# Kernel optimization log

Hardware: AMD Instinct MI355X
Metric: run time of the kernel (lower is better)

Reference implementation:

```python
import jax, jax.numpy as jnp
import numpy as np

N, E, IN, H, OUT = 100000, 1600000, 128, 128, 64


def setup_inputs() -> dict:
    key = jax.random.key(0)
    ks = jax.random.split(key, 6)
    glorot = lambda k, i, o: jax.random.normal(k, (i, o), jnp.float32) * np.float32(np.sqrt(2.0 / (i + o)))
    return dict(
        x=jax.random.normal(ks[0], (N, IN), jnp.float32),
        edge_index=jax.random.randint(ks[1], (2, E), 0, N, dtype=jnp.int64 if jax.config.jax_enable_x64 else jnp.int32),
        W1=glorot(ks[2], IN, H), b1=jnp.zeros((H,), jnp.float32),
        W2=glorot(ks[3], H, H), b2=jnp.zeros((H,), jnp.float32),
        W3=glorot(ks[4], H, OUT), b3=jnp.zeros((OUT,), jnp.float32),
    )


def _gcn_norm(edge_index, num_nodes):
    # add self loops with weight 1.0 (GCNConv add_self_loops=True, edge_weight=None -> ones)
    loop = jnp.arange(num_nodes, dtype=edge_index.dtype)
    src = jnp.concatenate([edge_index[0], loop])
    dst = jnp.concatenate([edge_index[1], loop])
    ew = jnp.ones(src.shape, jnp.float32)
    deg = jax.ops.segment_sum(ew, dst, num_segments=num_nodes)  # in-degree on dst
    dinv = jnp.where(deg > 0, jax.lax.rsqrt(deg), 0.0)
    norm = dinv[src] * ew * dinv[dst]  # [E+N]
    return src, dst, norm


def _conv(x, src, dst, norm, W, b):
    h = x @ W                                        # linear transform first (GCNConv order)
    msg = h[src] * norm[:, None]                     # gather + scale, [E+N, F]
    agg = jax.ops.segment_sum(msg, dst, num_segments=x.shape[0])  # scatter-add
    return agg + b


def reference(x, edge_index, W1, b1, W2, b2, W3, b3):
    # eval-mode forward: dropout is identity
    src, dst, norm = _gcn_norm(edge_index, x.shape[0])  # same graph -> norm shared across layers
    h = jax.nn.relu(_conv(x, src, dst, norm, W1, b1))
    h = jax.nn.relu(_conv(h, src, dst, norm, W2, b2))
    h = _conv(h, src, dst, norm, W3, b3)
    return jax.nn.log_softmax(h, axis=-1)
```

## Files before the change

### kernel.cpp

```cpp
#include <hip/hip_runtime.h>

typedef unsigned int u32;
typedef unsigned short u16;
typedef unsigned char u8;
typedef __attribute__((ext_vector_type(8))) short short8;
typedef __attribute__((ext_vector_type(4))) float f32x4;
typedef __attribute__((ext_vector_type(2))) float f32x2;

#define MAXBIN 1024

__device__ inline float bfu2f(u32 u) { return __builtin_bit_cast(float, u); }
__device__ inline u16 f2bf(float f) {
    u32 u = __builtin_bit_cast(u32, f);
    u32 r = (u + 0x7fffu + ((u >> 16) & 1u)) >> 16;
    return (u16)r;
}

__global__ __launch_bounds__(256) void k_bhist(const int* __restrict__ ei, int E, int W,
                                               int* __restrict__ binTot, int NBIN) {
    __shared__ int h[MAXBIN];
    int tid = threadIdx.x;
    for (int i = tid; i < NBIN; i += 256) h[i] = 0;
    __syncthreads();
    int s = blockIdx.x * W, e = min(E, s + W);
    for (int j = s + tid; j < e; j += 256) atomicAdd(&h[ei[E + j] >> 7], 1);
    __syncthreads();
    for (int i = tid; i < NBIN; i += 256) {
        int v = h[i];
        if (v) atomicAdd(&binTot[i], v);
    }
}

__global__ void k_bscan(const int* __restrict__ binTot, int NBIN,
                        int* __restrict__ binStart, int* __restrict__ binCur) {
    __shared__ int wsum[4];
    int t = threadIdx.x;
    int base = t * 4;
    int v0 = (base + 0 < NBIN) ? binTot[base + 0] : 0;
    int v1 = (base + 1 < NBIN) ? binTot[base + 1] : 0;
    int v2 = (base + 2 < NBIN) ? binTot[base + 2] : 0;
    int v3 = (base + 3 < NBIN) ? binTot[base + 3] : 0;
    int s = v0 + v1 + v2 + v3;
    int lane = t & 63, wv = t >> 6;
    int isc = s;
    for (int d = 1; d < 64; d <<= 1) { int o = __shfl_up(isc, d, 64); if (lane >= d) isc += o; }
    if (lane == 63) wsum[wv] = isc;
    __syncthreads();
    int woff = 0;
    for (int w = 0; w < wv; w++) woff += wsum[w];
    int run = woff + isc - s;
    if (base + 0 < NBIN) { binStart[base + 0] = run; binCur[base + 0] = run; } run += v0;
    if (base + 1 < NBIN) { binStart[base + 1] = run; binCur[base + 1] = run; } run += v1;
    if (base + 2 < NBIN) { binStart[base + 2] = run; binCur[base + 2] = run; } run += v2;
    if (base + 3 < NBIN) { binStart[base + 3] = run; binCur[base + 3] = run; }
    if (t == 255) binStart[NBIN] = wsum[0] + wsum[1] + wsum[2] + wsum[3];
}

__global__ __launch_bounds__(256) void k_bscatter(const int* __restrict__ ei, int E, int W,
                                                  int* __restrict__ binCur,
                                                  u32* __restrict__ binned, int NBIN) {
    __shared__ int lh[MAXBIN];
    __shared__ int lb[MAXBIN];
    int tid = threadIdx.x;
    for (int i = tid; i < NBIN; i += 256) lh[i] = 0;
    __syncthreads();
    int s = blockIdx.x * W, e = min(E, s + W);
    for (int j = s + tid; j < e; j += 256) atomicAdd(&lh[ei[E + j] >> 7], 1);
    __syncthreads();
    for (int i = tid; i < NBIN; i += 256) {
        int h = lh[i];
        lb[i] = h ? atomicAdd(&binCur[i], h) : 0;
    }
    __syncthreads();
    for (int i = tid; i < NBIN; i += 256) lh[i] = 0;
    __syncthreads();
    for (int j = s + tid; j < e; j += 256) {
        int d = ei[E + j];
        int b = d >> 7;
        int r = atomicAdd(&lh[b], 1);
        binned[lb[b] + r] = ((u32)ei[j] << 7) | (u32)(d & 127);
    }
}

__global__ __launch_bounds__(256) void k_bcsr(const u32* __restrict__ binned,
                                              const int* __restrict__ binStart,
                                              int N, int E, int* __restrict__ offs,
                                              float* __restrict__ dinv,
                                              int* __restrict__ csr, int NBIN) {
    __shared__ int cnt[128];
    __shared__ int off[128];
    __shared__ int tot;
    int b = blockIdx.x;
    int tid = threadIdx.x;
    int dLo = b << 7;
    int nd = min(128, N - dLo);
    int e0 = binStart[b], e1 = binStart[b + 1];
    if (tid < 128) cnt[tid] = 0;
    __syncthreads();
    for (int j = e0 + tid; j < e1; j += 256) atomicAdd(&cnt[binned[j] & 127u], 1);
    __syncthreads();
    int c = (tid < 128) ? cnt[tid] : 0;
    int lane = tid & 63;
    int isc = c;
    for (int d = 1; d < 64; d <<= 1) { int o = __shfl_up(isc, d, 64); if (lane >= d) isc += o; }
    if (tid == 63) tot = isc;
    __syncthreads();
    int add = (tid >= 64 && tid < 128) ? tot : 0;
    if (tid < 128) off[tid] = add + isc - c;
    __syncthreads();
    if (tid < nd) {
        offs[dLo + tid] = e0 + off[tid];
        dinv[dLo + tid] = rsqrtf((float)(c + 1));
    }
    if (b == NBIN - 1 && tid == 0) offs[N] = E;
    if (tid < 128) cnt[tid] = 0;
    __syncthreads();
    for (int j = e0 + tid; j < e1; j += 256) {
        u32 v = binned[j];
        int d7 = (int)(v & 127u);
        int r = atomicAdd(&cnt[d7], 1);
        csr[e0 + off[d7] + r] = (int)(v >> 7);
    }
}

__global__ void k_wtall(const float* __restrict__ W1, const float* __restrict__ W2,
                        const float* __restrict__ W3, u16* __restrict__ wt1,
                        u16* __restrict__ wt2, u16* __restrict__ wt3) {
    int idx = blockIdx.x * 256 + threadIdx.x;
    if (idx < 16384) {
        int k = idx >> 7, m = idx & 127;
        wt1[m * 128 + k] = f2bf(W1[idx]);
    } else if (idx < 32768) {
        int i = idx - 16384, k = i >> 7, m = i & 127;
        wt2[m * 128 + k] = f2bf(W2[i]);
    } else if (idx < 40960) {
        int i = idx - 32768, k = i >> 6, m = i & 63;
        wt3[m * 128 + k] = f2bf(W3[i]);
    }
}

template <int M, bool F32IN>
__global__ __launch_bounds__(256) void k_gemm(const void* __restrict__ xin,
                                              const u16* __restrict__ wt,
                                              const float* __restrict__ dinv,
                                              u8* __restrict__ g8, int N) {
    constexpr int K = 128;
    constexpr int LDK = 136;
    __shared__ u16 lwt[M * LDK];
    int tid = threadIdx.x;
    const uint4* wsrc = (const uint4*)wt;
#pragma unroll
    for (int c = tid; c < M * K / 8; c += 256) {
        int row = c >> 4, kc = c & 15;
        *(uint4*)&lwt[row * LDK + kc * 8] = wsrc[c];
    }
    __syncthreads();
    int lane = tid & 63, wv = tid >> 6;
    int node = blockIdx.x * 64 + wv * 16 + (lane & 15);
    int nodec = min(node, N - 1);
    int kr = (lane >> 4) * 8;
    f32x4 acc[M / 16];
#pragma unroll
    for (int t = 0; t < M / 16; t++) acc[t] = (f32x4){0.f, 0.f, 0.f, 0.f};
#pragma unroll
    for (int ks = 0; ks < 4; ks++) {
        short8 bfr;
        if (F32IN) {
            const float* xr = (const float*)xin + (size_t)nodec * K + ks * 32 + kr;
            float4 fa = *(const float4*)xr;
            float4 fb = *(const float4*)(xr + 4);
            bfr = (short8){(short)f2bf(fa.x), (short)f2bf(fa.y), (short)f2bf(fa.z),
                           (short)f2bf(fa.w), (short)f2bf(fb.x), (short)f2bf(fb.y),
                           (short)f2bf(fb.z), (short)f2bf(fb.w)};
        } else {
            bfr = *(const short8*)((const u16*)xin + (size_t)nodec * K + ks * 32 + kr);
        }
#pragma unroll
        for (int t = 0; t < M / 16; t++) {
            short8 afr = *(const short8*)&lwt[(t * 16 + (lane & 15)) * LDK + ks * 32 + kr];
            acc[t] = __builtin_amdgcn_mfma_f32_16x16x32_bf16(afr, bfr, acc[t], 0, 0, 0);
        }
    }
    if (node < N) {
        float dv16 = dinv[node] * 16.0f;
        int r0 = (lane >> 4) * 4;
#pragma unroll
        for (int t = 0; t < M / 16; t++) {
            u32 w = __builtin_amdgcn_cvt_pk_fp8_f32(acc[t][0] * dv16, acc[t][1] * dv16, 0, false);
            w = __builtin_amdgcn_cvt_pk_fp8_f32(acc[t][2] * dv16, acc[t][3] * dv16, w, true);
            *(u32*)(g8 + (size_t)node * M + t * 16 + r0) = w;
        }
    }
}

__global__ __launch_bounds__(256) void k_agg128(const u8* __restrict__ g8,
                                                const int* __restrict__ offs,
                                                const int* __restrict__ csr,
                                                const float* __restrict__ dinv,
                                                const float* __restrict__ bias,
                                                u16* __restrict__ hout, int N) {
    int wid = (blockIdx.x * 256 + threadIdx.x) >> 6;
    if (wid >= N) return;
    int lane = threadIdx.x & 63;
    int q = lane >> 4;
    int f = lane & 15;
    int s = offs[wid], e = offs[wid + 1];
    const u8* gf = g8 + f * 8;
    f32x2 a01 = {0.f, 0.f}, a23 = {0.f, 0.f}, a45 = {0.f, 0.f}, a67 = {0.f, 0.f};
    int em1 = e - 1;
    for (int j = s; j < e; j += 16) {
        int b4 = j + q * 4;
        int i1 = b4 + 1, i2 = b4 + 2, i3 = b4 + 3;
        int s0 = csr[min(b4, em1)];
        int s1 = csr[min(i1, em1)];
        int s2 = csr[min(i2, em1)];
        int s3 = csr[min(i3, em1)];
        uint2 w0 = *(const uint2*)(gf + ((u32)s0 << 7));
        uint2 w1 = *(const uint2*)(gf + ((u32)s1 << 7));
        uint2 w2 = *(const uint2*)(gf + ((u32)s2 << 7));
        uint2 w3 = *(const uint2*)(gf + ((u32)s3 << 7));
        if (b4 >= e) { w0.x = 0u; w0.y = 0u; }
        if (i1 >= e) { w1.x = 0u; w1.y = 0u; }
        if (i2 >= e) { w2.x = 0u; w2.y = 0u; }
        if (i3 >= e) { w3.x = 0u; w3.y = 0u; }
        f32x2 t0, t1;
        t0 = __builtin_amdgcn_cvt_pk_f32_fp8((int)w0.x, false) +
             __builtin_amdgcn_cvt_pk_f32_fp8((int)w1.x, false);
        t1 = __builtin_amdgcn_cvt_pk_f32_fp8((int)w2.x, false) +
             __builtin_amdgcn_cvt_pk_f32_fp8((int)w3.x, false);
        a01 += t0 + t1;
        t0 = __builtin_amdgcn_cvt_pk_f32_fp8((int)w0.x, true) +
             __builtin_amdgcn_cvt_pk_f32_fp8((int)w1.x, true);
        t1 = __builtin_amdgcn_cvt_pk_f32_fp8((int)w2.x, true) +
             __builtin_amdgcn_cvt_pk_f32_fp8((int)w3.x, true);
        a23 += t0 + t1;
        t0 = __builtin_amdgcn_cvt_pk_f32_fp8((int)w0.y, false) +
             __builtin_amdgcn_cvt_pk_f32_fp8((int)w1.y, false);
        t1 = __builtin_amdgcn_cvt_pk_f32_fp8((int)w2.y, false) +
             __builtin_amdgcn_cvt_pk_f32_fp8((int)w3.y, false);
        a45 += t0 + t1;
        t0 = __builtin_amdgcn_cvt_pk_f32_fp8((int)w0.y, true) +
             __builtin_amdgcn_cvt_pk_f32_fp8((int)w1.y, true);
        t1 = __builtin_amdgcn_cvt_pk_f32_fp8((int)w2.y, true) +
             __builtin_amdgcn_cvt_pk_f32_fp8((int)w3.y, true);
        a67 += t0 + t1;
    }
    float a[8] = {a01.x, a01.y, a23.x, a23.y, a45.x, a45.y, a67.x, a67.y};
#pragma unroll
    for (int i = 0; i < 8; i++) {
        a[i] += __shfl_xor(a[i], 16, 64);
        a[i] += __shfl_xor(a[i], 32, 64);
    }
    if (lane < 16) {
        float sc = dinv[wid] * 0.0625f;
        uint2 sp = *(const uint2*)(g8 + (size_t)wid * 128 + f * 8);
        f32x2 s01 = __builtin_amdgcn_cvt_pk_f32_fp8((int)sp.x, false);
        f32x2 s23 = __builtin_amdgcn_cvt_pk_f32_fp8((int)sp.x, true);
        f32x2 s45 = __builtin_amdgcn_cvt_pk_f32_fp8((int)sp.y, false);
        f32x2 s67 = __builtin_amdgcn_cvt_pk_f32_fp8((int)sp.y, true);
        float sv[8] = {s01.x, s01.y, s23.x, s23.y, s45.x, s45.y, s67.x, s67.y};
        float4 b0 = *(const float4*)(bias + f * 8);
        float4 b1 = *(const float4*)(bias + f * 8 + 4);
        float bv[8] = {b0.x, b0.y, b0.z, b0.w, b1.x, b1.y, b1.z, b1.w};
        u32 o[4];
#pragma unroll
        for (int i = 0; i < 4; i++) {
            float v0 = fmaxf(fmaf(a[2 * i] + sv[2 * i], sc, bv[2 * i]), 0.f);
            float v1 = fmaxf(fmaf(a[2 * i + 1] + sv[2 * i + 1], sc, bv[2 * i + 1]), 0.f);
            o[i] = (u32)f2bf(v0) | ((u32)f2bf(v1) << 16);
        }
        *(uint4*)&hout[(size_t)wid * 128 + f * 8] = make_uint4(o[0], o[1], o[2], o[3]);
    }
}

__global__ __launch_bounds__(256) void k_agg64(const u8* __restrict__ g8,
                                               const int* __restrict__ offs,
                                               const int* __restrict__ csr,
                                               const float* __restrict__ dinv,
                                               const float* __restrict__ bias,
                                               float* __restrict__ out, int N) {
    int wid = (blockIdx.x * 256 + threadIdx.x) >> 6;
    if (wid >= N) return;
    int lane = threadIdx.x & 63;
    int q = lane >> 4;
    int f = lane & 15;
    int s = offs[wid], e = offs[wid + 1];
    const u8* gf = g8 + f * 4;
    f32x2 a01 = {0.f, 0.f}, a23 = {0.f, 0.f};
    int em1 = e - 1;
    for (int j = s; j < e; j += 16) {
        int b4 = j + q * 4;
        int i1 = b4 + 1, i2 = b4 + 2, i3 = b4 + 3;
        int s0 = csr[min(b4, em1)];
        int s1 = csr[min(i1, em1)];
        int s2 = csr[min(i2, em1)];
        int s3 = csr[min(i3, em1)];
        u32 w0 = *(const u32*)(gf + ((u32)s0 << 6));
        u32 w1 = *(const u32*)(gf + ((u32)s1 << 6));
        u32 w2 = *(const u32*)(gf + ((u32)s2 << 6));
        u32 w3 = *(const u32*)(gf + ((u32)s3 << 6));
        if (b4 >= e) w0 = 0u;
        if (i1 >= e) w1 = 0u;
        if (i2 >= e) w2 = 0u;
        if (i3 >= e) w3 = 0u;
        f32x2 t0 = __builtin_amdgcn_cvt_pk_f32_fp8((int)w0, false) +
                   __builtin_amdgcn_cvt_pk_f32_fp8((int)w1, false);
        f32x2 t1 = __builtin_amdgcn_cvt_pk_f32_fp8((int)w2, false) +
                   __builtin_amdgcn_cvt_pk_f32_fp8((int)w3, false);
        a01 += t0 + t1;
        t0 = __builtin_amdgcn_cvt_pk_f32_fp8((int)w0, true) +
             __builtin_amdgcn_cvt_pk_f32_fp8((int)w1, true);
        t1 = __builtin_amdgcn_cvt_pk_f32_fp8((int)w2, true) +
             __builtin_amdgcn_cvt_pk_f32_fp8((int)w3, true);
        a23 += t0 + t1;
    }
    float a[4] = {a01.x, a01.y, a23.x, a23.y};
#pragma unroll
    for (int i = 0; i < 4; i++) {
        a[i] += __shfl_xor(a[i], 16, 64);
        a[i] += __shfl_xor(a[i], 32, 64);
    }
    if (lane < 16) {
        float sc = dinv[wid] * 0.0625f;
        u32 sp = *(const u32*)(g8 + (size_t)wid * 64 + f * 4);
        f32x2 s01 = __builtin_amdgcn_cvt_pk_f32_fp8((int)sp, false);
        f32x2 s23 = __builtin_amdgcn_cvt_pk_f32_fp8((int)sp, true);
        float4 bb = *(const float4*)(bias + f * 4);
        float v0 = fmaf(a[0] + s01.x, sc, bb.x);
        float v1 = fmaf(a[1] + s01.y, sc, bb.y);
        float v2 = fmaf(a[2] + s23.x, sc, bb.z);
        float v3 = fmaf(a[3] + s23.y, sc, bb.w);
        float m = fmaxf(fmaxf(v0, v1), fmaxf(v2, v3));
#pragma unroll
        for (int d = 8; d >= 1; d >>= 1) m = fmaxf(m, __shfl_xor(m, d, 64));
        float ssum = __expf(v0 - m) + __expf(v1 - m) + __expf(v2 - m) + __expf(v3 - m);
#pragma unroll
        for (int d = 8; d >= 1; d >>= 1) ssum += __shfl_xor(ssum, d, 64);
        float lg = m + __logf(ssum);
        *(float4*)&out[(size_t)wid * 64 + f * 4] =
            make_float4(v0 - lg, v1 - lg, v2 - lg, v3 - lg);
    }
}

extern "C" void kernel_launch(void* const* d_in, const int* in_sizes, int n_in,
                              void* d_out, int out_size, void* d_ws, size_t ws_size,
                              hipStream_t stream) {
    const float* x  = (const float*)d_in[0];
    const int*   ei = (const int*)d_in[1];
    const float* W1 = (const float*)d_in[2];
    const float* b1 = (const float*)d_in[3];
    const float* W2 = (const float*)d_in[4];
    const float* b2 = (const float*)d_in[5];
    const float* W3 = (const float*)d_in[6];
    const float* b3 = (const float*)d_in[7];
    const int N = in_sizes[0] / 128;
    const int E = in_sizes[1] / 2;
    const int NBIN = (N + 127) >> 7;

    char* ws = (char*)d_ws;
    size_t o = 0;
    auto alloc = [&](size_t bytes) -> char* {
        char* p = ws + o;
        o += (bytes + 255) & ~(size_t)255;
        return p;
    };
    int*   binTot = (int*)alloc((size_t)MAXBIN * 4);
    int*   binSt  = (int*)alloc((size_t)(MAXBIN + 1) * 4);
    int*   binCur = (int*)alloc((size_t)MAXBIN * 4);
    float* dinv   = (float*)alloc((size_t)N * 4);
    int*   offs   = (int*)alloc((size_t)(N + 1) * 4);
    int*   csr    = (int*)alloc((size_t)E * 4);
    u16*   wt1    = (u16*)alloc(128 * 128 * 2);
    u16*   wt2    = (u16*)alloc(128 * 128 * 2);
    u16*   wt3    = (u16*)alloc(64 * 128 * 2);
    u8*    g8     = (u8*)alloc((size_t)N * 128);
    u16*   hbuf   = (u16*)alloc((size_t)N * 128 * 2);
    u32*   binned = (u32*)hbuf;
    float* outp   = (float*)d_out;

    hipMemsetAsync(binTot, 0, (size_t)MAXBIN * 4, stream);
    int W256 = (E + 255) / 256;
    int W128 = (E + 127) / 128;
    k_bhist<<<256, 256, 0, stream>>>(ei, E, W256, binTot, NBIN);
    k_bscan<<<1, 256, 0, stream>>>(binTot, NBIN, binSt, binCur);
    k_bscatter<<<128, 256, 0, stream>>>(ei, E, W128, binCur, binned, NBIN);
    k_bcsr<<<NBIN, 256, 0, stream>>>(binned, binSt, N, E, offs, dinv, csr, NBIN);
    k_wtall<<<(40960 + 255) / 256, 256, 0, stream>>>(W1, W2, W3, wt1, wt2, wt3);

    int gG = (N + 63) / 64;
    int gA = (int)(((size_t)N * 64 + 255) / 256);

    k_gemm<128, true ><<<gG, 256, 0, stream>>>(x,    wt1, dinv, g8, N);
    k_agg128<<<gA, 256, 0, stream>>>(g8, offs, csr, dinv, b1, hbuf, N);
    k_gemm<128, false><<<gG, 256, 0, stream>>>(hbuf, wt2, dinv, g8, N);
    k_agg128<<<gA, 256, 0, stream>>>(g8, offs, csr, dinv, b2, hbuf, N);
    k_gemm<64,  false><<<gG, 256, 0, stream>>>(hbuf, wt3, dinv, g8, N);
    k_agg64<<<gA, 256, 0, stream>>>(g8, offs, csr, dinv, b3, outp, N);
}
```

Before: 346.8 us.

## Replace two-level binned CSR build with global-atomic degree count and scatter

Replaces the bucketed CSR construction (LDS histogram, bin scan, bin scatter, per-bin local sort) with a direct approach: global atomic degree counts, a two-pass block scan to compute row offsets, and a global-atomic scatter of source indices into CSR slots. This drops the intermediate binned array and a pass over the edges, but relies on contended global atomics across 100k nodes. The order of neighbours within a row becomes nondeterministic, which changes the float summation order in aggregation. k_offs assumes NB <= 256 for the block-prefix reduction.

```diff
diff --git a/kernel.cpp b/kernel.cpp
--- a/kernel.cpp
+++ b/kernel.cpp
@@ -7,8 +7,6 @@
 typedef __attribute__((ext_vector_type(4))) float f32x4;
 typedef __attribute__((ext_vector_type(2))) float f32x2;
 
-#define MAXBIN 1024
-
 __device__ inline float bfu2f(u32 u) { return __builtin_bit_cast(float, u); }
 __device__ inline u16 f2bf(float f) {
     u32 u = __builtin_bit_cast(u32, f);
@@ -16,111 +14,78 @@
     return (u16)r;
 }
 
-__global__ __launch_bounds__(256) void k_bhist(const int* __restrict__ ei, int E, int W,
-                                               int* __restrict__ binTot, int NBIN) {
-    __shared__ int h[MAXBIN];
-    int tid = threadIdx.x;
-    for (int i = tid; i < NBIN; i += 256) h[i] = 0;
+
+#define SCH 512
+
+__global__ __launch_bounds__(256) void k_deg(const int* __restrict__ ei, int E,
+                                             int* __restrict__ deg) {
+    int idx = blockIdx.x * 256 + threadIdx.x;
+    if (idx < E) atomicAdd(&deg[ei[E + idx]], 1);
+}
+
+__global__ __launch_bounds__(256) void k_scan1(const int* __restrict__ deg, int N,
+                                               int* __restrict__ psum) {
+    __shared__ int red[4];
+    int b = blockIdx.x, t = threadIdx.x;
+    int i0 = b * SCH + t * 2;
+    int s = 0;
+    if (i0 < N) s += deg[i0];
+    if (i0 + 1 < N) s += deg[i0 + 1];
+#pragma unroll
+    for (int d = 1; d < 64; d <<= 1) s += __shfl_xor(s, d, 64);
+    if ((t & 63) == 0) red[t >> 6] = s;
     __syncthreads();
-    int s = blockIdx.x * W, e = min(E, s + W);
-    for (int j = s + tid; j < e; j += 256) atomicAdd(&h[ei[E + j] >> 7], 1);
+    if (t == 0) psum[b] = red[0] + red[1] + red[2] + red[3];
+}
+
+__global__ __launch_bounds__(256) void k_offs(const int* __restrict__ deg,
+                                              const int* __restrict__ psum,
+                                              int N, int E, int NB,
+                                              int* __restrict__ offs,
+                                              int* __restrict__ cur,
+                                              float* __restrict__ dinv) {
+    __shared__ int red[4];
+    __shared__ int wsum[4];
+    __shared__ int pblk;
+    int b = blockIdx.x, t = threadIdx.x;
+    int lane = t & 63, wv = t >> 6;
+    int pv = (t < b && t < NB) ? psum[t] : 0;
+#pragma unroll
+    for (int d = 1; d < 64; d <<= 1) pv += __shfl_xor(pv, d, 64);
+    if (lane == 0) red[wv] = pv;
     __syncthreads();
-    for (int i = tid; i < NBIN; i += 256) {
-        int v = h[i];
-        if (v) atomicAdd(&binTot[i], v);
-    }
-}
-
-__global__ void k_bscan(const int* __restrict__ binTot, int NBIN,
-                        int* __restrict__ binStart, int* __restrict__ binCur) {
-    __shared__ int wsum[4];
-    int t = threadIdx.x;
-    int base = t * 4;
-    int v0 = (base + 0 < NBIN) ? binTot[base + 0] : 0;
-    int v1 = (base + 1 < NBIN) ? binTot[base + 1] : 0;
-    int v2 = (base + 2 < NBIN) ? binTot[base + 2] : 0;
-    int v3 = (base + 3 < NBIN) ? binTot[base + 3] : 0;
-    int s = v0 + v1 + v2 + v3;
-    int lane = t & 63, wv = t >> 6;
+    if (t == 0) pblk = red[0] + red[1] + red[2] + red[3];
+    int i0 = b * SCH + t * 2;
+    int v0 = (i0 < N) ? deg[i0] : 0;
+    int v1 = (i0 + 1 < N) ? deg[i0 + 1] : 0;
+    int s = v0 + v1;
     int isc = s;
+#pragma unroll
     for (int d = 1; d < 64; d <<= 1) { int o = __shfl_up(isc, d, 64); if (lane >= d) isc += o; }
     if (lane == 63) wsum[wv] = isc;
     __syncthreads();
-    int woff = 0;
+    int woff = pblk;
     for (int w = 0; w < wv; w++) woff += wsum[w];
-    int run = woff + isc - s;
-    if (base + 0 < NBIN) { binStart[base + 0] = run; binCur[base + 0] = run; } run += v0;
-    if (base + 1 < NBIN) { binStart[base + 1] = run; binCur[base + 1] = run; } run += v1;
-    if (base + 2 < NBIN) { binStart[base + 2] = run; binCur[base + 2] = run; } run += v2;
-    if (base + 3 < NBIN) { binStart[base + 3] = run; binCur[base + 3] = run; }
-    if (t == 255) binStart[NBIN] = wsum[0] + wsum[1] + wsum[2] + wsum[3];
-}
-
-__global__ __launch_bounds__(256) void k_bscatter(const int* __restrict__ ei, int E, int W,
-                                                  int* __restrict__ binCur,
-                                                  u32* __restrict__ binned, int NBIN) {
-    __shared__ int lh[MAXBIN];
-    __shared__ int lb[MAXBIN];
-    int tid = threadIdx.x;
-    for (int i = tid; i < NBIN; i += 256) lh[i] = 0;
-    __syncthreads();
-    int s = blockIdx.x * W, e = min(E, s + W);
-    for (int j = s + tid; j < e; j += 256) atomicAdd(&lh[ei[E + j] >> 7], 1);
-    __syncthreads();
-    for (int i = tid; i < NBIN; i += 256) {
-        int h = lh[i];
-        lb[i] = h ? atomicAdd(&binCur[i], h) : 0;
-    }
-    __syncthreads();
-    for (int i = tid; i < NBIN; i += 256) lh[i] = 0;
-    __syncthreads();
-    for (int j = s + tid; j < e; j += 256) {
-        int d = ei[E + j];
-        int b = d >> 7;
-        int r = atomicAdd(&lh[b], 1);
-        binned[lb[b] + r] = ((u32)ei[j] << 7) | (u32)(d & 127);
-    }
-}
-
-__global__ __launch_bounds__(256) void k_bcsr(const u32* __restrict__ binned,
-                                              const int* __restrict__ binStart,
-                                              int N, int E, int* __restrict__ offs,
-                                              float* __restrict__ dinv,
-                                              int* __restrict__ csr, int NBIN) {
-    __shared__ int cnt[128];
-    __shared__ int off[128];
-    __shared__ int tot;
-    int b = blockIdx.x;
-    int tid = threadIdx.x;
-    int dLo = b << 7;
-    int nd = min(128, N - dLo);
-    int e0 = binStart[b], e1 = binStart[b + 1];
-    if (tid < 128) cnt[tid] = 0;
-    __syncthreads();
-    for (int j = e0 + tid; j < e1; j += 256) atomicAdd(&cnt[binned[j] & 127u], 1);
-    __syncthreads();
-    int c = (tid < 128) ? cnt[tid] : 0;
-    int lane = tid & 63;
-    int isc = c;
-    for (int d = 1; d < 64; d <<= 1) { int o = __shfl_up(isc, d, 64); if (lane >= d) isc += o; }
-    if (tid == 63) tot = isc;
-    __syncthreads();
-    int add = (tid >= 64 && tid < 128) ? tot : 0;
-    if (tid < 128) off[tid] = add + isc - c;
-    __syncthreads();
-    if (tid < nd) {
-        offs[dLo + tid] = e0 + off[tid];
-        dinv[dLo + tid] = rsqrtf((float)(c + 1));
-    }
-    if (b == NBIN - 1 && tid == 0) offs[N] = E;
-    if (tid < 128) cnt[tid] = 0;
-    __syncthreads();
-    for (int j = e0 + tid; j < e1; j += 256) {
-        u32 v = binned[j];
-        int d7 = (int)(v & 127u);
-        int r = atomicAdd(&cnt[d7], 1);
-        csr[e0 + off[d7] + r] = (int)(v >> 7);
-    }
+    int ex = woff + isc - s;
+    if (i0 < N) {
+        offs[i0] = ex; cur[i0] = ex;
+        dinv[i0] = rsqrtf((float)(v0 + 1));
+    }
+    if (i0 + 1 < N) {
+        offs[i0 + 1] = ex + v0; cur[i0 + 1] = ex + v0;
+        dinv[i0 + 1] = rsqrtf((float)(v1 + 1));
+    }
+    if (b == 0 && t == 0) offs[N] = E;
+}
+
+__global__ __launch_bounds__(256) void k_scatter(const int* __restrict__ ei, int E,
+                                                 int* __restrict__ cur,
+                                                 int* __restrict__ csr) {
+    int idx = blockIdx.x * 256 + threadIdx.x;
+    if (idx >= E) return;
+    int d = ei[E + idx];
+    int r = atomicAdd(&cur[d], 1);
+    csr[r] = ei[idx];
 }
 
 __global__ void k_wtall(const float* __restrict__ W1, const float* __restrict__ W2,
@@ -355,7 +320,7 @@
     const float* b3 = (const float*)d_in[7];
     const int N = in_sizes[0] / 128;
     const int E = in_sizes[1] / 2;
-    const int NBIN = (N + 127) >> 7;
+    const int NB = (N + SCH - 1) / SCH;
 
     char* ws = (char*)d_ws;
     size_t o = 0;
@@ -364,9 +329,9 @@
         o += (bytes + 255) & ~(size_t)255;
         return p;
     };
-    int*   binTot = (int*)alloc((size_t)MAXBIN * 4);
-    int*   binSt  = (int*)alloc((size_t)(MAXBIN + 1) * 4);
-    int*   binCur = (int*)alloc((size_t)MAXBIN * 4);
+    int*   deg    = (int*)alloc((size_t)N * 4);
+    int*   psum   = (int*)alloc(256 * 4);
+    int*   cur    = (int*)alloc((size_t)N * 4);
     float* dinv   = (float*)alloc((size_t)N * 4);
     int*   offs   = (int*)alloc((size_t)(N + 1) * 4);
     int*   csr    = (int*)alloc((size_t)E * 4);
@@ -375,16 +340,14 @@
     u16*   wt3    = (u16*)alloc(64 * 128 * 2);
     u8*    g8     = (u8*)alloc((size_t)N * 128);
     u16*   hbuf   = (u16*)alloc((size_t)N * 128 * 2);
-    u32*   binned = (u32*)hbuf;
     float* outp   = (float*)d_out;
 
-    hipMemsetAsync(binTot, 0, (size_t)MAXBIN * 4, stream);
-    int W256 = (E + 255) / 256;
-    int W128 = (E + 127) / 128;
-    k_bhist<<<256, 256, 0, stream>>>(ei, E, W256, binTot, NBIN);
-    k_bscan<<<1, 256, 0, stream>>>(binTot, NBIN, binSt, binCur);
-    k_bscatter<<<128, 256, 0, stream>>>(ei, E, W128, binCur, binned, NBIN);
-    k_bcsr<<<NBIN, 256, 0, stream>>>(binned, binSt, N, E, offs, dinv, csr, NBIN);
+    hipMemsetAsync(deg, 0, (size_t)N * 4, stream);
+    int gE = (E + 255) / 256;
+    k_deg<<<gE, 256, 0, stream>>>(ei, E, deg);
+    k_scan1<<<NB, 256, 0, stream>>>(deg, N, psum);
+    k_offs<<<NB, 256, 0, stream>>>(deg, psum, N, E, NB, offs, cur, dinv);
+    k_scatter<<<gE, 256, 0, stream>>>(ei, E, cur, csr);
     k_wtall<<<(40960 + 255) / 256, 256, 0, stream>>>(W1, W2, W3, wt1, wt2, wt3);
 
     int gG = (N + 63) / 64;
```

After: 467.6 us. 34.8% more time.
